# Performance work log

Hardware: AMD Instinct MI355X
Metric: run time of the kernel (lower is better)

## Reference

```python
import jax, jax.numpy as jnp
import numpy as np

B, S, E = 2, 2048, 2048
H, KV, D = 16, 4, 128
G = H // KV  # query heads per kv head
THETA = 10000.0


def setup_inputs() -> dict:
    key = jax.random.key(0)
    ks = jax.random.split(key, 5)
    scale = 0.02
    return {
        "x": jax.random.normal(ks[0], (B, S, E), dtype=jnp.float32),
        "Wq": jax.random.normal(ks[1], (E, H * D), dtype=jnp.float32) * scale,
        "Wk": jax.random.normal(ks[2], (E, KV * D), dtype=jnp.float32) * scale,
        "Wv": jax.random.normal(ks[3], (E, KV * D), dtype=jnp.float32) * scale,
        "Wo": jax.random.normal(ks[4], (E, E), dtype=jnp.float32) * scale,
    }


def _rope_tables(seq_len, head_dim, theta):
    inv_freq = 1.0 / theta ** (jnp.arange(0, head_dim, 2, dtype=jnp.float32) / head_dim)
    t = jnp.arange(seq_len, dtype=jnp.float32)
    freqs = jnp.outer(t, inv_freq)  # [S, D/2]
    cos = jnp.concatenate([jnp.cos(freqs), jnp.cos(freqs)], axis=-1)  # [S, D]
    sin = jnp.concatenate([jnp.sin(freqs), jnp.sin(freqs)], axis=-1)
    return cos, sin


def _apply_rope(x, cos, sin):
    # x: [B, h, S, D]; cos/sin: [S, D] broadcast over batch/heads
    d2 = x.shape[-1] // 2
    x1, x2 = x[..., :d2], x[..., d2:]
    rotated = jnp.concatenate([-x2, x1], axis=-1)
    return x * cos + rotated * sin


def reference(x, Wq, Wk, Wv, Wo):
    b, s, _ = x.shape
    q = (x @ Wq).reshape(b, s, H, D).transpose(0, 2, 1, 3)   # [B,H,S,D]
    k = (x @ Wk).reshape(b, s, KV, D).transpose(0, 2, 1, 3)  # [B,KV,S,D]
    v = (x @ Wv).reshape(b, s, KV, D).transpose(0, 2, 1, 3)

    cos, sin = _rope_tables(s, D, THETA)
    q = _apply_rope(q, cos, sin)
    k = _apply_rope(k, cos, sin)

    # GQA: q head h attends to kv head h // G (repeat_interleave order)
    qg = q.reshape(b, KV, G, s, D)
    scores = jnp.einsum("bkgsd,bktd->bkgst", qg, k) / jnp.sqrt(jnp.asarray(D, x.dtype))
    causal = jnp.tril(jnp.ones((s, s), dtype=bool))
    scores = jnp.where(causal, scores, jnp.asarray(-jnp.inf, scores.dtype))
    attn = jax.nn.softmax(scores, axis=-1)
    out = jnp.einsum("bkgst,bktd->bkgsd", attn, v)  # [B,KV,G,S,D]
    out = out.reshape(b, H, s, D).transpose(0, 2, 1, 3).reshape(b, s, H * D)
    return out @ Wo
```

## Files before the change

### kernel.cpp

```cpp
#include <hip/hip_runtime.h>
#include <stdint.h>

#define B_ 2
#define S_ 2048
#define E_ 2048
#define H_ 16
#define KV_ 4
#define D_ 128
#define G_ (H_ / KV_)
#define M_ (B_ * S_)

typedef unsigned short u16;
typedef unsigned int u32;
typedef __bf16 bf16x8 __attribute__((ext_vector_type(8)));
typedef float f32x4 __attribute__((ext_vector_type(4)));

__device__ __forceinline__ u16 f2bf(float f) {
  __bf16 h = (__bf16)f;
  return *(u16*)&h;
}
__device__ __forceinline__ float bf2f(u16 x) {
  return __uint_as_float(((u32)x) << 16);
}
__device__ __forceinline__ void store_c(u16* p, float v) { *p = f2bf(v); }
__device__ __forceinline__ void store_c(float* p, float v) { *p = v; }

__device__ __forceinline__ void gload_lds16(const u16* g, u16* lds) {
  __builtin_amdgcn_global_load_lds((const __attribute__((address_space(1))) u32*)g,
                                   (__attribute__((address_space(3))) u32*)lds,
                                   16, 0, 0);
}

__global__ __launch_bounds__(256) void convert_fp32_bf16(const float4* __restrict__ x,
                                                         uint2* __restrict__ o, int n4) {
  int i = blockIdx.x * 256 + threadIdx.x;
  if (i >= n4) return;
  float4 v = x[i];
  uint2 r;
  r.x = (u32)f2bf(v.x) | ((u32)f2bf(v.y) << 16);
  r.y = (u32)f2bf(v.z) | ((u32)f2bf(v.w) << 16);
  o[i] = r;
}

__global__ __launch_bounds__(256) void transpose_conv_w(const float* __restrict__ W,
                                                        u16* __restrict__ Wt,
                                                        int Kdim, int Ndim) {
  __shared__ float tile[32][33];
  int n0 = blockIdx.x * 32, k0 = blockIdx.y * 32;
  int tx = threadIdx.x, ty = threadIdx.y;
#pragma unroll
  for (int i = 0; i < 4; i++) {
    int r = ty + i * 8;
    tile[r][tx] = W[(size_t)(k0 + r) * Ndim + n0 + tx];
  }
  __syncthreads();
#pragma unroll
  for (int i = 0; i < 4; i++) {
    int r = ty + i * 8;
    Wt[(size_t)(n0 + r) * Kdim + k0 + tx] = f2bf(tile[tx][r]);
  }
}

__global__ __launch_bounds__(256) void transpose_v(const u16* __restrict__ V,
                                                   u16* __restrict__ Vt) {
  __shared__ u16 tile[32][33];
  int bkv = blockIdx.z;
  int b = bkv / KV_, kv = bkv % KV_;
  int s0 = blockIdx.x * 32, d0 = blockIdx.y * 32;
  int tx = threadIdx.x, ty = threadIdx.y;
#pragma unroll
  for (int i = 0; i < 4; i++) {
    int r = ty + i * 8;
    tile[r][tx] = V[((size_t)((b * S_ + s0 + r) * KV_ + kv)) * D_ + d0 + tx];
  }
  __syncthreads();
#pragma unroll
  for (int i = 0; i < 4; i++) {
    int r = ty + i * 8;
    Vt[((size_t)(b * KV_ + kv) * D_ + d0 + r) * S_ + s0 + tx] = tile[tx][r];
  }
}

__global__ __launch_bounds__(256) void rope_k_repack(const u16* __restrict__ Kin,
                                                     u16* __restrict__ Kp, int total) {
  int idx = blockIdx.x * 256 + threadIdx.x;
  if (idx >= total) return;
  int d = idx & 63;
  int rem = idx >> 6;
  int kv = rem % KV_;
  int row = rem / KV_;
  int b = row >> 11;
  int spos = row & (S_ - 1);
  size_t src = ((size_t)row * KV_ + kv) * D_ + d;
  float x0 = bf2f(Kin[src]);
  float x1 = bf2f(Kin[src + 64]);
  float ang = (float)spos * expf(-0.14391156831212787f * (float)d);
  float sn, cs;
  sincosf(ang, &sn, &cs);
  size_t dst = ((size_t)((b * KV_ + kv) * S_ + spos)) * D_ + d;
  Kp[dst]      = f2bf(x0 * cs - x1 * sn);
  Kp[dst + 64] = f2bf(x1 * cs + x0 * sn);
}

template <typename CT>
__device__ __forceinline__ void gemm256_body(const u16* __restrict__ A,
                                             const u16* __restrict__ Bt,
                                             CT* __restrict__ C,
                                             int Kdim, int Ndim, int m0, int n0) {
  extern __shared__ __align__(16) u16 smem[];
  const int tid  = threadIdx.x;
  const int lane = tid & 63;
  const int wave = tid >> 6;
  const int wm   = wave >> 2;
  const int wn   = wave & 3;
  const int bh   = wn >> 1;
  const int nb   = (wn & 1) * 64;
  const int quad = lane >> 4, lm = lane & 15;

  int soff[2], sldb[2];
#pragma unroll
  for (int i = 0; i < 2; i++) {
    int cc  = i * 512 + tid;
    int row = cc >> 3;
    int q   = (cc & 7) ^ (row & 7);
    soff[i] = row * Kdim + q * 8;
    sldb[i] = (i * 512 + wave * 64) * 8;
  }
  auto STAGE = [&](const u16* g, u16* l) {
    gload_lds16(g + soff[0], l + sldb[0]);
    gload_lds16(g + soff[1], l + sldb[1]);
  };

  int cs0 = ((0 + quad) ^ (lm & 7)) * 8;
  int cs1 = ((4 + quad) ^ (lm & 7)) * 8;

  const u16* Ag = A  + (size_t)m0 * Kdim;
  const u16* Bg = Bt + (size_t)n0 * Kdim;
  const size_t hstep = (size_t)128 * Kdim;

  f32x4 acc[8][4];
  f32x4 zero = {0.f, 0.f, 0.f, 0.f};
#pragma unroll
  for (int m = 0; m < 8; m++)
#pragma unroll
    for (int n = 0; n < 4; n++) acc[m][n] = zero;

  const int NKT = Kdim >> 6;

  STAGE(Bg,             smem + 32768 + 0 * 8192);
  STAGE(Ag,             smem + 0 * 8192);
  STAGE(Ag + hstep,     smem + 1 * 8192);
  STAGE(Bg + hstep,     smem + 32768 + 1 * 8192);
  STAGE(Bg + 64,        smem + 32768 + 2 * 8192);
  STAGE(Ag + 64,        smem + 2 * 8192);
  STAGE(Ag + hstep + 64, smem + 3 * 8192);
  asm volatile("s_waitcnt vmcnt(6)" ::: "memory");
  __builtin_amdgcn_s_barrier();

  for (int kt = 0; kt < NKT; ++kt) {
    const int cur = kt & 1;
    const u16* regA = smem + (cur * 2 + wm) * 8192;
    const u16* regB = smem + 32768 + (cur * 2 + bh) * 8192;
    bf16x8 af[4][2], bf[4][2];

#pragma unroll
    for (int n = 0; n < 4; n++) {
      bf[n][0] = *(const bf16x8*)(regB + (nb + n * 16 + lm) * 64 + cs0);
      bf[n][1] = *(const bf16x8*)(regB + (nb + n * 16 + lm) * 64 + cs1);
    }
#pragma unroll
    for (int m = 0; m < 4; m++) {
      af[m][0] = *(const bf16x8*)(regA + (m * 16 + lm) * 64 + cs0);
      af[m][1] = *(const bf16x8*)(regA + (m * 16 + lm) * 64 + cs1);
    }
    if (kt + 1 < NKT)
      STAGE(Bg + hstep + (size_t)(kt + 1) * 64,
            smem + 32768 + (((kt + 1) & 1) * 2 + 1) * 8192);
    asm volatile("s_waitcnt lgkmcnt(0)" ::: "memory");
    __builtin_amdgcn_s_barrier();
    __builtin_amdgcn_s_setprio(1);
#pragma unroll
    for (int m = 0; m < 4; m++)
#pragma unroll
      for (int n = 0; n < 2; n++) {
        acc[m][n] = __builtin_amdgcn_mfma_f32_16x16x32_bf16(af[m][0], bf[n][0], acc[m][n], 0, 0, 0);
        acc[m][n] = __builtin_amdgcn_mfma_f32_16x16x32_bf16(af[m][1], bf[n][1], acc[m][n], 0, 0, 0);
      }
    __builtin_amdgcn_s_setprio(0);
    __builtin_amdgcn_s_barrier();

    if (kt + 2 < NKT)
      STAGE(Bg + (size_t)(kt + 2) * 64, smem + 32768 + (cur * 2 + 0) * 8192);
    __builtin_amdgcn_s_barrier();
    __builtin_amdgcn_s_setprio(1);
#pragma unroll
    for (int m = 0; m < 4; m++)
#pragma unroll
      for (int n = 2; n < 4; n++) {
        acc[m][n] = __builtin_amdgcn_mfma_f32_16x16x32_bf16(af[m][0], bf[n][0], acc[m][n], 0, 0, 0);
        acc[m][n] = __builtin_amdgcn_mfma_f32_16x16x32_bf16(af[m][1], bf[n][1], acc[m][n], 0, 0, 0);
      }
    __builtin_amdgcn_s_setprio(0);
    __builtin_amdgcn_s_barrier();

#pragma unroll
    for (int m = 0; m < 4; m++) {
      af[m][0] = *(const bf16x8*)(regA + ((m + 4) * 16 + lm) * 64 + cs0);
      af[m][1] = *(const bf16x8*)(regA + ((m + 4) * 16 + lm) * 64 + cs1);
    }
    asm volatile("s_waitcnt lgkmcnt(0)" ::: "memory");
    __builtin_amdgcn_s_barrier();
    __builtin_amdgcn_s_setprio(1);
#pragma unroll
    for (int m = 0; m < 4; m++)
#pragma unroll
      for (int n = 0; n < 2; n++) {
        acc[m + 4][n] = __builtin_amdgcn_mfma_f32_16x16x32_bf16(af[m][0], bf[n][0], acc[m + 4][n], 0, 0, 0);
        acc[m + 4][n] = __builtin_amdgcn_mfma_f32_16x16x32_bf16(af[m][1], bf[n][1], acc[m + 4][n], 0, 0, 0);
      }
    __builtin_amdgcn_s_setprio(0);
    __builtin_amdgcn_s_barrier();

    if (kt + 2 < NKT) {
      STAGE(Ag + (size_t)(kt + 2) * 64,         smem + (cur * 2 + 0) * 8192);
      STAGE(Ag + hstep + (size_t)(kt + 2) * 64, smem + (cur * 2 + 1) * 8192);
    }
    __builtin_amdgcn_s_setprio(1);
#pragma unroll
    for (int m = 0; m < 4; m++)
#pragma unroll
      for (int n = 2; n < 4; n++) {
        acc[m + 4][n] = __builtin_amdgcn_mfma_f32_16x16x32_bf16(af[m][0], bf[n][0], acc[m + 4][n], 0, 0, 0);
        acc[m + 4][n] = __builtin_amdgcn_mfma_f32_16x16x32_bf16(af[m][1], bf[n][1], acc[m + 4][n], 0, 0, 0);
      }
    __builtin_amdgcn_s_setprio(0);
    asm volatile("s_waitcnt vmcnt(6)" ::: "memory");
    __builtin_amdgcn_s_barrier();
  }

#pragma unroll
  for (int m = 0; m < 8; m++) {
    const int row = m0 + wm * 128 + m * 16 + quad * 4;
#pragma unroll
    for (int n = 0; n < 4; n++) {
      const int col = n0 + wn * 64 + n * 16 + lm;
#pragma unroll
      for (int r = 0; r < 4; r++)
        store_c(C + (size_t)(row + r) * Ndim + col, acc[m][n][r]);
    }
  }
}

__global__ __launch_bounds__(512, 2) void gemm256_qkv(const u16* __restrict__ A,
                                                      const u16* __restrict__ WqT,
                                                      const u16* __restrict__ WkT,
                                                      const u16* __restrict__ WvT,
                                                      u16* __restrict__ Qb,
                                                      u16* __restrict__ Kb,
                                                      u16* __restrict__ Vb) {
  int bx = blockIdx.x;
  const u16* Bt;
  u16* C;
  int n0, Ndim;
  if (bx < 8)       { Bt = WqT; C = Qb; n0 = bx * 256;        Ndim = 2048; }
  else if (bx < 10) { Bt = WkT; C = Kb; n0 = (bx - 8) * 256;  Ndim = 512; }
  else              { Bt = WvT; C = Vb; n0 = (bx - 10) * 256; Ndim = 512; }
  gemm256_body<u16>(A, Bt, C, 2048, Ndim, blockIdx.y * 256, n0);
}

__global__ __launch_bounds__(512, 2) void gemm256_wo(const u16* __restrict__ A,
                                                     const u16* __restrict__ Bt,
                                                     float* __restrict__ C) {
  gemm256_body<float>(A, Bt, C, 2048, 2048, blockIdx.y * 256, blockIdx.x * 256);
}

__global__ __launch_bounds__(512, 2) void attn_kernel(const u16* __restrict__ Q,
                                                      const u16* __restrict__ Kp,
                                                      const u16* __restrict__ Vt,
                                                      u16* __restrict__ O) {
  __shared__ __align__(16) u16 Ksh[2][64 * 128];
  __shared__ __align__(16) u16 Vsh[2][128 * 64];
  __shared__ __align__(16) u16 Psh[8][16 * 64];

  const int tid = threadIdx.x;
  const int lane = tid & 63;
  const int wave = tid >> 6;
  const int quad = lane >> 4, lm = lane & 15;
  const int b = blockIdx.z, h = blockIdx.x;
  const int kh = h / G_;

  const u16* Kbase = Kp + (size_t)(b * KV_ + kh) * S_ * D_;
  const u16* Vbase = Vt + (size_t)(b * KV_ + kh) * D_ * S_;
  u16* pw = &Psh[wave][0];

  int offK[2], offV[2], ldsOff[2];
#pragma unroll
  for (int i = 0; i < 2; i++) {
    int idx = (wave * 2 + i) * 64 + lane;
    int rK = idx >> 4;
    int cK = (idx & 15) ^ (rK & 7);
    offK[i] = rK * 128 + cK * 8;
    int rV = idx >> 3;
    int cV = (idx & 7) ^ (rV & 7);
    offV[i] = rV * S_ + cV * 8;
    ldsOff[i] = (wave * 2 + i) * 512;
  }

  bf16x8 onesb;
#pragma unroll
  for (int j = 0; j < 8; j++) onesb[j] = (__bf16)1.0f;

#pragma unroll
  for (int half = 0; half < 2; half++) {
    const int qi = half ? blockIdx.y : (15 - blockIdx.y);
    const int sq0 = qi * 128;
    const int nT = 2 * qi + 2;
    const int wrow = sq0 + wave * 16;

    const int spos = wrow + lm;
    const u16* qptr = Q + ((size_t)(b * S_ + wrow + lm) * H_ + h) * D_;
    bf16x8 qf[4];
#pragma unroll
    for (int ks = 0; ks < 2; ks++) {
      bf16x8 a = *(const bf16x8*)(qptr + ks * 32 + quad * 8);
      bf16x8 c = *(const bf16x8*)(qptr + (ks + 2) * 32 + quad * 8);
#pragma unroll
      for (int j = 0; j < 8; j++) {
        int d = ks * 32 + quad * 8 + j;
        float ang = (float)spos * __expf(-0.14391156831212787f * (float)d);
        float sn, cs;
        sincosf(ang, &sn, &cs);
        float x0 = (float)a[j], x1 = (float)c[j];
        const float scale = 0.08838834764831845f;
        qf[ks][j]     = (__bf16)((x0 * cs - x1 * sn) * scale);
        qf[ks + 2][j] = (__bf16)((x1 * cs + x0 * sn) * scale);
      }
    }

    f32x4 o[8];
    f32x4 lacc = {0.f, 0.f, 0.f, 0.f};
#pragma unroll
    for (int i = 0; i < 8; i++) o[i] = f32x4{0.f, 0.f, 0.f, 0.f};

    __syncthreads();

#pragma unroll
    for (int i = 0; i < 2; i++)
      gload_lds16(Kbase + offK[i], &Ksh[0][ldsOff[i]]);
#pragma unroll
    for (int i = 0; i < 2; i++)
      gload_lds16(Vbase + offV[i], &Vsh[0][ldsOff[i]]);

    for (int t = 0; t < nT; t++) {
      const int sk0 = t << 6;
      const bool act = (sk0 <= wrow + 15);

      __builtin_amdgcn_s_barrier();

      if (t + 1 < nT) {
        const u16* kg = Kbase + (size_t)(t + 1) * 64 * 128;
        const u16* vg = Vbase + (t + 1) * 64;
        u16* kb_next = &Ksh[(t + 1) & 1][0];
        u16* vb_next = &Vsh[(t + 1) & 1][0];
#pragma unroll
        for (int i = 0; i < 2; i++)
          gload_lds16(kg + offK[i], kb_next + ldsOff[i]);
#pragma unroll
        for (int i = 0; i < 2; i++)
          gload_lds16(vg + offV[i], vb_next + ldsOff[i]);
        asm volatile("s_waitcnt vmcnt(4)" ::: "memory");
      } else {
        asm volatile("s_waitcnt vmcnt(0)" ::: "memory");
      }

      __builtin_amdgcn_s_barrier();
      __builtin_amdgcn_sched_barrier(0);

      if (act) {
        const u16* kbuf = &Ksh[t & 1][0];
        f32x4 sc[4];
#pragma unroll
        for (int nt = 0; nt < 4; nt++) sc[nt] = f32x4{0.f, 0.f, 0.f, 0.f};
        __builtin_amdgcn_s_setprio(1);
#pragma unroll
        for (int ks = 0; ks < 4; ks++) {
#pragma unroll
          for (int nt = 0; nt < 4; nt++) {
            int R = nt * 16 + lm;
            bf16x8 kb = *(const bf16x8*)(kbuf + R * 128 + (((ks * 4 + quad) ^ (R & 7)) * 8));
            sc[nt] = __builtin_amdgcn_mfma_f32_16x16x32_bf16(qf[ks], kb, sc[nt], 0, 0, 0);
          }
        }
        __builtin_amdgcn_s_setprio(0);
#pragma unroll
        for (int nt = 0; nt < 4; nt++)
#pragma unroll
          for (int r = 0; r < 4; r++) {
            float p = __expf(sc[nt][r]);
            int kc = sk0 + nt * 16 + lm;
            int qr = wrow + quad * 4 + r;
            sc[nt][r] = (kc > qr) ? 0.f : p;
          }
#pragma unroll
        for (int nt = 0; nt < 4; nt++)
#pragma unroll
          for (int r = 0; r < 4; r++) {
            int p = quad * 4 + r;
            int c = nt * 2 + (lm >> 3);
            pw[p * 64 + ((c ^ (p & 7)) * 8) + (lm & 7)] = f2bf(sc[nt][r]);
          }
        const u16* vbuf = &Vsh[t & 1][0];
        __builtin_amdgcn_s_setprio(1);
#pragma unroll
        for (int ks = 0; ks < 2; ks++) {
          int pr = lm;
          bf16x8 pa = *(const bf16x8*)(pw + pr * 64 + (((ks * 4 + quad) ^ (pr & 7)) * 8));
          lacc = __builtin_amdgcn_mfma_f32_16x16x32_bf16(pa, onesb, lacc, 0, 0, 0);
#pragma unroll
          for (int d8 = 0; d8 < 8; d8++) {
            int R = d8 * 16 + lm;
            bf16x8 vb = *(const bf16x8*)(vbuf + R * 64 + (((ks * 4 + quad) ^ (R & 7)) * 8));
            o[d8] = __builtin_amdgcn_mfma_f32_16x16x32_bf16(pa, vb, o[d8], 0, 0, 0);
          }
        }
        __builtin_amdgcn_s_setprio(0);
      }
    }

    float inv[4];
#pragma unroll
    for (int r = 0; r < 4; r++) inv[r] = 1.0f / lacc[r];
#pragma unroll
    for (int d8 = 0; d8 < 8; d8++)
#pragma unroll
      for (int r = 0; r < 4; r++) {
        int srow = wrow + quad * 4 + r;
        O[((size_t)(b * S_ + srow) * H_ + h) * D_ + d8 * 16 + lm] = f2bf(o[d8][r] * inv[r]);
      }
  }
}

extern "C" void kernel_launch(void* const* d_in, const int* in_sizes, int n_in,
                              void* d_out, int out_size, void* d_ws, size_t ws_size,
                              hipStream_t stream) {
  const float* x  = (const float*)d_in[0];
  const float* Wq = (const float*)d_in[1];
  const float* Wk = (const float*)d_in[2];
  const float* Wv = (const float*)d_in[3];
  const float* Wo = (const float*)d_in[4];
  float* out = (float*)d_out;
  char* ws = (char*)d_ws;
  u16* Xb  = (u16*)(ws);
  u16* WqT = (u16*)(ws + (16ull << 20));
  u16* WkT = (u16*)(ws + (24ull << 20));
  u16* WvT = (u16*)(ws + (26ull << 20));
  u16* WoT = (u16*)(ws + (28ull << 20));
  u16* Qb  = (u16*)(ws + (36ull << 20));
  u16* Kb  = (u16*)(ws + (52ull << 20));
  u16* Vb  = (u16*)(ws + (56ull << 20));
  u16* Vt  = (u16*)(ws + (60ull << 20));
  u16* Ob  = (u16*)(ws + (64ull << 20));
  u16* Kp  = (u16*)(ws + (80ull << 20));

  static bool attr_set = false;
  if (!attr_set) {
    hipFuncSetAttribute((const void*)gemm256_qkv,
                        hipFuncAttributeMaxDynamicSharedMemorySize, 131072);
    hipFuncSetAttribute((const void*)gemm256_wo,
                        hipFuncAttributeMaxDynamicSharedMemorySize, 131072);
    attr_set = true;
  }

  dim3 tb32(32, 8);

  convert_fp32_bf16<<<dim3(M_ * E_ / 4 / 256), 256, 0, stream>>>((const float4*)x, (uint2*)Xb, M_ * E_ / 4);
  transpose_conv_w<<<dim3(2048 / 32, 2048 / 32), tb32, 0, stream>>>(Wq, WqT, E_, H_ * D_);
  transpose_conv_w<<<dim3(512 / 32, 2048 / 32), tb32, 0, stream>>>(Wk, WkT, E_, KV_ * D_);
  transpose_conv_w<<<dim3(512 / 32, 2048 / 32), tb32, 0, stream>>>(Wv, WvT, E_, KV_ * D_);
  transpose_conv_w<<<dim3(2048 / 32, 2048 / 32), tb32, 0, stream>>>(Wo, WoT, E_, E_);

  gemm256_qkv<<<dim3(12, M_ / 256), 512, 131072, stream>>>(Xb, WqT, WkT, WvT, Qb, Kb, Vb);

  rope_k_repack<<<dim3(M_ * KV_ * 64 / 256), 256, 0, stream>>>(Kb, Kp, M_ * KV_ * 64);

  transpose_v<<<dim3(S_ / 32, D_ / 32, B_ * KV_), tb32, 0, stream>>>(Vb, Vt);

  attn_kernel<<<dim3(H_, 8, B_), 512, 0, stream>>>(Qb, Kp, Vt, Ob);

  gemm256_wo<<<dim3(2048 / 256, M_ / 256), 512, 131072, stream>>>(Ob, WoT, out);
}
```

Before: 316.4 us.

## Split causal attention KV range across twice as many blocks with partial-sum combine

Doubles the attention grid so that each block handles one KV segment for each of two paired query tiles, chosen so the per-block work stays balanced. Each block writes unnormalized fp32 output partials and row sums, and a new combine kernel adds the two partials and normalizes to bf16. The aim is better CU utilisation across 256 CUs. The cost is an extra kernel launch and tens of MB of extra fp32 traffic. Raising launch bounds to 4 blocks per CU tightens the register budget and may cause spills, while LDS use likely still caps residency at 2 blocks per CU.

New measurement: 342.0 us. 1.08x slower.

```diff
diff --git a/kernel.cpp b/kernel.cpp
--- a/kernel.cpp
+++ b/kernel.cpp
@@ -274,10 +274,13 @@
   gemm256_body<float>(A, Bt, C, 2048, 2048, blockIdx.y * 256, blockIdx.x * 256);
 }
 
-__global__ __launch_bounds__(512, 2) void attn_kernel(const u16* __restrict__ Q,
+__global__ __launch_bounds__(512, 4) void attn_kernel(const u16* __restrict__ Q,
                                                       const u16* __restrict__ Kp,
                                                       const u16* __restrict__ Vt,
-                                                      u16* __restrict__ O) {
+                                                      float* __restrict__ Of0,
+                                                      float* __restrict__ Of1,
+                                                      float* __restrict__ Lf0,
+                                                      float* __restrict__ Lf1) {
   __shared__ __align__(16) u16 Ksh[2][64 * 128];
   __shared__ __align__(16) u16 Vsh[2][128 * 64];
   __shared__ __align__(16) u16 Psh[8][16 * 64];
@@ -287,6 +290,7 @@
   const int wave = tid >> 6;
   const int quad = lane >> 4, lm = lane & 15;
   const int b = blockIdx.z, h = blockIdx.x;
+  const int j = blockIdx.y;
   const int kh = h / G_;
 
   const u16* Kbase = Kp + (size_t)(b * KV_ + kh) * S_ * D_;
@@ -308,13 +312,14 @@
 
   bf16x8 onesb;
 #pragma unroll
-  for (int j = 0; j < 8; j++) onesb[j] = (__bf16)1.0f;
-
-#pragma unroll
-  for (int half = 0; half < 2; half++) {
-    const int qi = half ? blockIdx.y : (15 - blockIdx.y);
+  for (int jj = 0; jj < 8; jj++) onesb[jj] = (__bf16)1.0f;
+
+#pragma unroll
+  for (int seg = 0; seg < 2; seg++) {
+    const int qi = seg ? j : (15 - j);
+    const int t0 = seg ? (j + 1) : 0;
+    const int t1 = seg ? (2 * j + 2) : (16 - j);
     const int sq0 = qi * 128;
-    const int nT = 2 * qi + 2;
     const int wrow = sq0 + wave * 16;
 
     const int spos = wrow + lm;
@@ -325,15 +330,15 @@
       bf16x8 a = *(const bf16x8*)(qptr + ks * 32 + quad * 8);
       bf16x8 c = *(const bf16x8*)(qptr + (ks + 2) * 32 + quad * 8);
 #pragma unroll
-      for (int j = 0; j < 8; j++) {
-        int d = ks * 32 + quad * 8 + j;
+      for (int jj = 0; jj < 8; jj++) {
+        int d = ks * 32 + quad * 8 + jj;
         float ang = (float)spos * __expf(-0.14391156831212787f * (float)d);
         float sn, cs;
         sincosf(ang, &sn, &cs);
-        float x0 = (float)a[j], x1 = (float)c[j];
+        float x0 = (float)a[jj], x1 = (float)c[jj];
         const float scale = 0.08838834764831845f;
-        qf[ks][j]     = (__bf16)((x0 * cs - x1 * sn) * scale);
-        qf[ks + 2][j] = (__bf16)((x1 * cs + x0 * sn) * scale);
+        qf[ks][jj]     = (__bf16)((x0 * cs - x1 * sn) * scale);
+        qf[ks + 2][jj] = (__bf16)((x1 * cs + x0 * sn) * scale);
       }
     }
 
@@ -346,18 +351,18 @@
 
 #pragma unroll
     for (int i = 0; i < 2; i++)
-      gload_lds16(Kbase + offK[i], &Ksh[0][ldsOff[i]]);
+      gload_lds16(Kbase + (size_t)t0 * 64 * 128 + offK[i], &Ksh[t0 & 1][ldsOff[i]]);
 #pragma unroll
     for (int i = 0; i < 2; i++)
-      gload_lds16(Vbase + offV[i], &Vsh[0][ldsOff[i]]);
-
-    for (int t = 0; t < nT; t++) {
+      gload_lds16(Vbase + t0 * 64 + offV[i], &Vsh[t0 & 1][ldsOff[i]]);
+
+    for (int t = t0; t < t1; t++) {
       const int sk0 = t << 6;
       const bool act = (sk0 <= wrow + 15);
 
       __builtin_amdgcn_s_barrier();
 
-      if (t + 1 < nT) {
+      if (t + 1 < t1) {
         const u16* kg = Kbase + (size_t)(t + 1) * 64 * 128;
         const u16* vg = Vbase + (t + 1) * 64;
         u16* kb_next = &Ksh[(t + 1) & 1][0];
@@ -427,17 +432,39 @@
       }
     }
 
-    float inv[4];
-#pragma unroll
-    for (int r = 0; r < 4; r++) inv[r] = 1.0f / lacc[r];
+    float* Os = seg ? Of1 : Of0;
+    float* Ls = seg ? Lf1 : Lf0;
 #pragma unroll
     for (int d8 = 0; d8 < 8; d8++)
 #pragma unroll
       for (int r = 0; r < 4; r++) {
         int srow = wrow + quad * 4 + r;
-        O[((size_t)(b * S_ + srow) * H_ + h) * D_ + d8 * 16 + lm] = f2bf(o[d8][r] * inv[r]);
-      }
-  }
+        Os[((size_t)(b * S_ + srow) * H_ + h) * D_ + d8 * 16 + lm] = o[d8][r];
+      }
+    if (lm == 0) {
+#pragma unroll
+      for (int r = 0; r < 4; r++) {
+        int srow = wrow + quad * 4 + r;
+        Ls[(size_t)(b * S_ + srow) * H_ + h] = lacc[r];
+      }
+    }
+  }
+}
+
+__global__ __launch_bounds__(256) void combine_o(const float4* __restrict__ Of0,
+                                                 const float4* __restrict__ Of1,
+                                                 const float* __restrict__ Lf0,
+                                                 const float* __restrict__ Lf1,
+                                                 uint2* __restrict__ Ob) {
+  int idx = blockIdx.x * 256 + threadIdx.x;
+  int rh = idx >> 5;
+  float4 a = Of0[idx];
+  float4 c = Of1[idx];
+  float inv = 1.0f / (Lf0[rh] + Lf1[rh]);
+  uint2 r;
+  r.x = (u32)f2bf((a.x + c.x) * inv) | ((u32)f2bf((a.y + c.y) * inv) << 16);
+  r.y = (u32)f2bf((a.z + c.z) * inv) | ((u32)f2bf((a.w + c.w) * inv) << 16);
+  Ob[idx] = r;
 }
 
 extern "C" void kernel_launch(void* const* d_in, const int* in_sizes, int n_in,
@@ -461,6 +488,10 @@
   u16* Vt  = (u16*)(ws + (60ull << 20));
   u16* Ob  = (u16*)(ws + (64ull << 20));
   u16* Kp  = (u16*)(ws + (80ull << 20));
+  float* Of0 = (float*)(ws + (84ull << 20));
+  float* Of1 = (float*)(ws + (116ull << 20));
+  float* Lf0 = (float*)(ws + (52ull << 20));
+  float* Lf1 = (float*)(ws + (53ull << 20));
 
   static bool attr_set = false;
   if (!attr_set) {
@@ -485,7 +516,10 @@
 
   transpose_v<<<dim3(S_ / 32, D_ / 32, B_ * KV_), tb32, 0, stream>>>(Vb, Vt);
 
-  attn_kernel<<<dim3(H_, 8, B_), 512, 0, stream>>>(Qb, Kp, Vt, Ob);
+  attn_kernel<<<dim3(H_, 16, B_), 512, 0, stream>>>(Qb, Kp, Vt, Of0, Of1, Lf0, Lf1);
+
+  combine_o<<<dim3(M_ * H_ * D_ / 4 / 256), 256, 0, stream>>>((const float4*)Of0, (const float4*)Of1,
+                                                              Lf0, Lf1, (uint2*)Ob);
 
   gemm256_wo<<<dim3(2048 / 256, M_ / 256), 512, 131072, stream>>>(Ob, WoT, out);
 }
```
